# Kernel optimization log

Measured on AMD Instinct MI355X. Metric: run time of the kernel, lower is better.

Reference implementation:

```python
import jax, jax.numpy as jnp
import numpy as np


def _gcn_layer(x, row, col, W, b):
    # x: [N, d_in]; row/col: [E'] (with self loops already appended)
    N = x.shape[0]
    deg = jax.ops.segment_sum(jnp.ones_like(row, dtype=x.dtype), row, num_segments=N)
    deg_inv_sqrt = deg ** -0.5  # self loops guarantee deg >= 1
    norm = deg_inv_sqrt[row] * deg_inv_sqrt[col]  # [E']
    msg = norm[:, None] * x[row]                  # gather + normalize
    aggr = jax.ops.segment_sum(msg, col, num_segments=N)  # scatter-add
    return aggr @ W + b


def reference(x, edge_index, W1, b1, W2, b2):
    N = x.shape[0]
    loops = jnp.arange(N, dtype=edge_index.dtype)
    row = jnp.concatenate([edge_index[0], loops])
    col = jnp.concatenate([edge_index[1], loops])
    h = jax.nn.relu(_gcn_layer(x, row, col, W1, b1))
    # F.dropout(training=self.training) is identity in eval mode
    out = _gcn_layer(h, row, col, W2, b2)
    return jax.nn.log_softmax(out, axis=1)


def setup_inputs() -> dict:
    key = jax.random.key(0)
    k1, k2, k3, k4 = jax.random.split(key, 4)
    N, E, F_IN, F_HID, F_OUT = 100000, 1200000, 64, 64, 16
    x = jax.random.normal(k1, (N, F_IN), dtype=jnp.float32)
    edge_index = jax.random.randint(k2, (2, E), 0, N, dtype=jnp.int64)
    W1 = jax.random.normal(k3, (F_IN, F_HID), dtype=jnp.float32) / np.sqrt(F_IN)
    b1 = jnp.zeros((F_HID,), dtype=jnp.float32)
    W2 = jax.random.normal(k4, (F_HID, F_OUT), dtype=jnp.float32) / np.sqrt(F_HID)
    b2 = jnp.zeros((F_OUT,), dtype=jnp.float32)
    return {"x": x, "edge_index": edge_index, "W1": W1, "b1": b1, "W2": W2, "b2": b2}
```

## Files before the change

### kernel.cpp

```cpp
#include <hip/hip_runtime.h>
#include <hip/hip_bf16.h>

typedef __attribute__((ext_vector_type(8))) _Float16 hfrag;
typedef __attribute__((ext_vector_type(4))) float ffrag;
typedef __attribute__((ext_vector_type(4))) _Float16 h4v;

#define BSH 8
#define LBS 256
#define CAP_SH 14
#define CAP (1 << CAP_SH)
#define NF 512
#define OPAD 520
#define CONV_BLKS 384
#define EPBC 4096
#define ELC 4096

__device__ __forceinline__ float b2f_(unsigned short u) {
    return __uint_as_float(((unsigned)u) << 16);
}
__device__ __forceinline__ unsigned short f2b_(float v) {
    __hip_bfloat16 h = __float2bfloat16(v);
    return *reinterpret_cast<unsigned short*>(&h);
}
__device__ __forceinline__ unsigned short f2h_(float v) {
    _Float16 h = (_Float16)v;
    return __builtin_bit_cast(unsigned short, h);
}
__device__ __forceinline__ float h2f_(unsigned short u) {
    _Float16 h = __builtin_bit_cast(_Float16, u);
    return (float)h;
}

__device__ __forceinline__ float loadF(const void* p, long long i, int isF32) {
    if (isF32) return ((const float*)p)[i];
    return b2f_(((const unsigned short*)p)[i]);
}

__device__ __forceinline__ float4 loadF4(const void* p, long long base, int i4, int isF32) {
    if (isF32) {
        return ((const float4*)((const float*)p + base))[i4];
    } else {
        ushort4 u = ((const ushort4*)((const unsigned short*)p + base))[i4];
        return make_float4(b2f_(u.x), b2f_(u.y), b2f_(u.z), b2f_(u.w));
    }
}

__device__ __forceinline__ void get_edge(const int* ei, int i64, int e, int E, int& s, int& d) {
    if (i64) { s = ei[2 * (long long)e]; d = ei[2 * (long long)E + 2 * (long long)e]; }
    else     { s = ei[e];                d = ei[(long long)E + e]; }
}

struct E4 { int s[4]; int d[4]; };
__device__ __forceinline__ E4 load4(const int* __restrict__ ei, int i64, int e0, int E) {
    E4 r;
    if (i64) {
        const int4* ps = (const int4*)(ei + 2 * (long long)e0);
        const int4* pd = (const int4*)(ei + 2 * (long long)E + 2 * (long long)e0);
        int4 a = ps[0], b = ps[1];
        int4 c = pd[0], d = pd[1];
        r.s[0] = a.x; r.s[1] = a.z; r.s[2] = b.x; r.s[3] = b.z;
        r.d[0] = c.x; r.d[1] = c.z; r.d[2] = d.x; r.d[3] = d.z;
    } else {
        int4 a = *(const int4*)(ei + e0);
        int4 c = *(const int4*)(ei + (long long)E + e0);
        r.s[0] = a.x; r.s[1] = a.y; r.s[2] = a.z; r.s[3] = a.w;
        r.d[0] = c.x; r.d[1] = c.y; r.d[2] = c.z; r.d[3] = c.w;
    }
    return r;
}

__device__ __forceinline__ void wave_scan_excl(int* a, int nEl, int lane) {
    int run = 0;
    for (int base = 0; base < nEl; base += 64) {
        int i = base + lane;
        int orig = (i < nEl) ? a[i] : 0;
        int v = orig;
#pragma unroll
        for (int off = 1; off < 64; off <<= 1) {
            int u = __shfl_up(v, off);
            if (lane >= off) v += u;
        }
        if (i < nEl) a[i] = v - orig + run;
        run += __shfl(v, 63);
    }
}

__global__ __launch_bounds__(256) void k_stage(const void* __restrict__ x,
                                               const int* __restrict__ ei,
                                               const void* __restrict__ W1, const void* __restrict__ b1,
                                               const void* __restrict__ W2, const void* __restrict__ b2,
                                               int E, int N, int nbk, int EPB,
                                               int* __restrict__ flags, float* __restrict__ Wbuf,
                                               unsigned short* __restrict__ Wh1,
                                               unsigned short* __restrict__ Wh2,
                                               int* __restrict__ off_d, int* __restrict__ off_s,
                                               int* __restrict__ pdst,
                                               unsigned char* __restrict__ psrc,
                                               unsigned short* __restrict__ xh) {
    __shared__ int hd[512], hs[512], cd[512], cs[512];
    __shared__ int es[EPBC], ed[EPBC];
    __shared__ int s_sane, s_zero;
    int tid = threadIdx.x;
    if (tid == 0) { s_sane = 0; s_zero = 0; }
    __syncthreads();
    const unsigned short* xu = (const unsigned short*)x;
    if (blockIdx.x == NF) {
        int sane = 0;
        for (int k = tid; k < 4096; k += 256) {
            float v = b2f_(xu[2 * k]);
            float a = fabsf(v);
            if (v == 0.0f || (a >= 9.3e-10f && a <= 1.1e9f)) sane++;
        }
        if (sane) atomicAdd(&s_sane, sane);
        int zero = 0;
        for (int k = tid; k < 1024; k += 256) if (ei[2 * k + 1] == 0) zero++;
        if (zero) atomicAdd(&s_zero, zero);
        __syncthreads();
        int f = (s_sane < 3000) ? 1 : 0;
        if (tid == 0) { flags[0] = f; flags[1] = (s_zero > 512) ? 1 : 0; }
        for (int i = tid; i < 4096; i += 256) Wbuf[i] = loadF(W1, i, f);
        if (tid < 64) Wbuf[4096 + tid] = loadF(b1, tid, f);
        for (int i = tid; i < 1024; i += 256) Wbuf[4160 + i] = loadF(W2, i, f);
        if (tid < 16) Wbuf[5184 + tid] = loadF(b2, tid, f);
        __syncthreads();
        for (int i = tid; i < 4096; i += 256) {
            int j = i & 7, m = (i >> 3) & 15, q = (i >> 7) & 3, kn = i >> 9;
            int kt = kn & 1, nt = kn >> 1;
            Wh1[i] = f2h_(Wbuf[(kt * 32 + q * 8 + j) * 64 + nt * 16 + m]);
        }
        for (int i = tid; i < 1024; i += 256) {
            int j = i & 7, m = (i >> 3) & 15, q = (i >> 7) & 3, kt = i >> 9;
            Wh2[i] = f2h_(Wbuf[4160 + (kt * 32 + q * 8 + j) * 16 + m]);
        }
        return;
    }
    if (blockIdx.x > NF) {
        int cb = blockIdx.x - NF - 1;
        int sane = 0;
        for (int k = tid; k < 4096; k += 256) {
            float v = b2f_(xu[2 * k]);
            float a = fabsf(v);
            if (v == 0.0f || (a >= 9.3e-10f && a <= 1.1e9f)) sane++;
        }
        if (sane) atomicAdd(&s_sane, sane);
        __syncthreads();
        int f = (s_sane < 3000) ? 1 : 0;
        int n4 = N * 16;
        int ctid = cb * 256 + tid;
        int stride = CONV_BLKS * 256 * 2;
        for (int i0 = ctid * 2; i0 < n4; i0 += stride) {
            float4 v0 = loadF4(x, 0, i0, f);
            float4 v1 = (i0 + 1 < n4) ? loadF4(x, 0, i0 + 1, f) : make_float4(0, 0, 0, 0);
            ushort4 o0, o1;
            o0.x = f2h_(v0.x); o0.y = f2h_(v0.y); o0.z = f2h_(v0.z); o0.w = f2h_(v0.w);
            o1.x = f2h_(v1.x); o1.y = f2h_(v1.y); o1.z = f2h_(v1.z); o1.w = f2h_(v1.w);
            ((ushort4*)xh)[i0] = o0;
            if (i0 + 1 < n4) ((ushort4*)xh)[i0 + 1] = o1;
        }
        return;
    }
    int zero = 0;
    for (int k = tid; k < 1024; k += 256) if (ei[2 * k + 1] == 0) zero++;
    if (zero) atomicAdd(&s_zero, zero);
    for (int i = tid; i < 512; i += 256) { hd[i] = 0; hs[i] = 0; }
    __syncthreads();
    int i64 = (s_zero > 512) ? 1 : 0;
    int fb = blockIdx.x;
    int elo = fb * EPB;
    int ehi = min(elo + EPB, E);
    if (elo >= E) {
        for (int b = tid; b <= nbk; b += 256) {
            off_d[fb * OPAD + b] = E; off_s[fb * OPAD + b] = E;
        }
        return;
    }
    int ecnt = ehi - elo;
    int rem = ecnt & 3, ebase = elo + (ecnt & ~3);
    if (ecnt <= EPBC) {
        for (int e0 = elo + tid * 4; e0 + 4 <= ehi; e0 += 1024) {
            E4 a = load4(ei, i64, e0, E);
            int base = e0 - elo;
#pragma unroll
            for (int u = 0; u < 4; ++u) { es[base + u] = a.s[u]; ed[base + u] = a.d[u]; }
        }
        if (tid < rem) {
            int s, d;
            get_edge(ei, i64, ebase + tid, E, s, d);
            es[ecnt - rem + tid] = s; ed[ecnt - rem + tid] = d;
        }
        __syncthreads();
        for (int i = tid; i < ecnt; i += 256) {
            atomicAdd(&hd[ed[i] >> BSH], 1);
            atomicAdd(&hs[es[i] >> BSH], 1);
        }
        __syncthreads();
        if (tid < 64)       wave_scan_excl(hd, nbk, tid);
        else if (tid < 128) wave_scan_excl(hs, nbk, tid - 64);
        __syncthreads();
        for (int b = tid; b < nbk; b += 256) {
            int od = elo + hd[b], os = elo + hs[b];
            off_d[fb * OPAD + b] = od; cd[b] = od;
            off_s[fb * OPAD + b] = os; cs[b] = os;
        }
        if (tid == 0) { off_d[fb * OPAD + nbk] = elo + ecnt; off_s[fb * OPAD + nbk] = elo + ecnt; }
        __syncthreads();
        for (int i = tid; i < ecnt; i += 256) {
            int s = es[i], d = ed[i];
            int p = atomicAdd(&cd[d >> BSH], 1);
            pdst[p] = (s << BSH) | (d & (LBS - 1));
            int q = atomicAdd(&cs[s >> BSH], 1);
            psrc[q] = (unsigned char)(s & (LBS - 1));
        }
        return;
    }
    for (int e0 = elo + tid * 4; e0 + 4 <= ehi; e0 += 1024) {
        E4 a = load4(ei, i64, e0, E);
#pragma unroll
        for (int u = 0; u < 4; ++u) {
            atomicAdd(&hd[a.d[u] >> BSH], 1);
            atomicAdd(&hs[a.s[u] >> BSH], 1);
        }
    }
    if (tid < rem) {
        int s, d;
        get_edge(ei, i64, ebase + tid, E, s, d);
        atomicAdd(&hd[d >> BSH], 1);
        atomicAdd(&hs[s >> BSH], 1);
    }
    __syncthreads();
    if (tid < 64)       wave_scan_excl(hd, nbk, tid);
    else if (tid < 128) wave_scan_excl(hs, nbk, tid - 64);
    __syncthreads();
    for (int b = tid; b < nbk; b += 256) {
        int od = elo + hd[b], os = elo + hs[b];
        off_d[fb * OPAD + b] = od; cd[b] = od;
        off_s[fb * OPAD + b] = os; cs[b] = os;
    }
    if (tid == 0) { off_d[fb * OPAD + nbk] = elo + ecnt; off_s[fb * OPAD + nbk] = elo + ecnt; }
    __syncthreads();
    for (int e0 = elo + tid * 4; e0 + 4 <= ehi; e0 += 1024) {
        E4 a = load4(ei, i64, e0, E);
#pragma unroll
        for (int u = 0; u < 4; ++u) {
            int p = atomicAdd(&cd[a.d[u] >> BSH], 1);
            pdst[p] = (a.s[u] << BSH) | (a.d[u] & (LBS - 1));
            int q = atomicAdd(&cs[a.s[u] >> BSH], 1);
            psrc[q] = (unsigned char)(a.s[u] & (LBS - 1));
        }
    }
    if (tid < rem) {
        int s, d;
        get_edge(ei, i64, ebase + tid, E, s, d);
        int p = atomicAdd(&cd[d >> BSH], 1);
        pdst[p] = (s << BSH) | (d & (LBS - 1));
        int q = atomicAdd(&cs[s >> BSH], 1);
        psrc[q] = (unsigned char)(s & (LBS - 1));
    }
}

__global__ __launch_bounds__(512) void k_degcsr(const unsigned char* __restrict__ psrc,
                                                const int* __restrict__ pdst,
                                                const int* __restrict__ off_s,
                                                const int* __restrict__ off_d,
                                                float* __restrict__ dis,
                                                int4* __restrict__ rdesc,
                                                int* __restrict__ psr, int N, int nbk) {
    __shared__ int elist[ELC];
    __shared__ int h[LBS], lb[LBS], cur[LBS];
    __shared__ float dloc[LBS];
    __shared__ int s_cnt;
    int b = blockIdx.x, tid = threadIdx.x;
    if (tid == 0) s_cnt = 0;
    if (tid < LBS) h[tid] = 0;
    __syncthreads();
    for (int fb = tid; fb < NF; fb += 512) {
        int o0 = off_s[fb * OPAD + b];
        int o1 = off_s[fb * OPAD + b + 1];
        for (int p = o0; p < o1; ++p) atomicAdd(&h[psrc[p]], 1);
    }
    __syncthreads();
    if (tid < LBS) {
        float dv = rsqrtf((float)h[tid] + 1.0f);
        dloc[tid] = dv;
        int node = b * LBS + tid;
        if (node < N) dis[node] = dv;
    }
    __syncthreads();
    if (tid < LBS) h[tid] = 0;
    __syncthreads();
    for (int fb = tid; fb < NF; fb += 512) {
        int o0 = off_d[fb * OPAD + b];
        int o1 = off_d[fb * OPAD + b + 1];
        int len = o1 - o0;
        if (len > 0) {
            int base = atomicAdd(&s_cnt, len);
            for (int k = 0; k < len; ++k)
                if (base + k < ELC) elist[base + k] = pdst[o0 + k];
        }
    }
    __syncthreads();
    int cnt = s_cnt;
    int beg = b << CAP_SH;
    if (cnt <= ELC) {
        for (int i = tid; i < cnt; i += 512) atomicAdd(&h[elist[i] & (LBS - 1)], 1);
        __syncthreads();
        if (tid < LBS) lb[tid] = h[tid];
        __syncthreads();
        if (tid < 64) wave_scan_excl(lb, LBS, tid);
        __syncthreads();
        if (tid < LBS) {
            cur[tid] = lb[tid];
            int node = b * LBS + tid;
            if (node < N) {
                int s0 = min(lb[tid], CAP), s1 = min(lb[tid] + h[tid], CAP);
                rdesc[node] = make_int4(beg + s0, beg + s1, __float_as_int(dloc[tid]), 0);
            }
        }
        __syncthreads();
        for (int i = tid; i < cnt; i += 512) {
            int e = elist[i];
            int r = atomicAdd(&cur[e & (LBS - 1)], 1);
            if (r < CAP) psr[beg + r] = e >> BSH;
        }
        return;
    }
    if (tid < LBS) h[tid] = 0;
    __syncthreads();
    for (int fb = tid; fb < NF; fb += 512) {
        int o0 = off_d[fb * OPAD + b];
        int o1 = off_d[fb * OPAD + b + 1];
        for (int p = o0; p < o1; ++p) atomicAdd(&h[pdst[p] & (LBS - 1)], 1);
    }
    __syncthreads();
    if (tid < LBS) lb[tid] = h[tid];
    __syncthreads();
    if (tid < 64) wave_scan_excl(lb, LBS, tid);
    __syncthreads();
    if (tid < LBS) {
        cur[tid] = lb[tid];
        int node = b * LBS + tid;
        if (node < N) {
            int s0 = min(lb[tid], CAP), s1 = min(lb[tid] + h[tid], CAP);
            rdesc[node] = make_int4(beg + s0, beg + s1, __float_as_int(dloc[tid]), 0);
        }
    }
    __syncthreads();
    for (int fb = tid; fb < NF; fb += 512) {
        int o0 = off_d[fb * OPAD + b];
        int o1 = off_d[fb * OPAD + b + 1];
        for (int p = o0; p < o1; ++p) {
            int e = pdst[p];
            int r = atomicAdd(&cur[e & (LBS - 1)], 1);
            if (r < CAP) psr[beg + r] = e >> BSH;
        }
    }
}

__global__ __launch_bounds__(256) void k_aggdense(const unsigned short* __restrict__ xh,
                                                  const float* __restrict__ dis,
                                                  const int4* __restrict__ rdesc,
                                                  const int* __restrict__ psr,
                                                  const unsigned short* __restrict__ Wh1,
                                                  const unsigned short* __restrict__ Wh2,
                                                  const float* __restrict__ Wbuf,
                                                  unsigned short* __restrict__ t2b, int N) {
    __shared__ __align__(16) unsigned short T[16 * 72];
    int tid = threadIdx.x;
    int lane = tid & 63;
    int w = tid >> 6;
    int g = lane >> 4, i4 = lane & 15;
    int ln = w * 4 + g;
    int n = blockIdx.x * 16 + ln;
    int act = (n < N);
    float4 A[4];
#pragma unroll
    for (int u = 0; u < 4; ++u) A[u] = make_float4(0.f, 0.f, 0.f, 0.f);
    float dd = 0.f;
    int beg = 0, end = 0;
    if (act) {
        int4 rd = rdesc[n];
        beg = rd.x; end = rd.y; dd = __int_as_float(rd.z);
        h4v xv = *(const h4v*)(xh + (long long)n * 64 + i4 * 4);
        float ww = dd * dd;
        A[0].x = ww * (float)xv[0]; A[0].y = ww * (float)xv[1];
        A[0].z = ww * (float)xv[2]; A[0].w = ww * (float)xv[3];
    }
    int cnt = end - beg;
    int Tn = (cnt + 7) >> 3;
    int p = beg;
    int e[8];
#pragma unroll
    for (int u = 0; u < 8; ++u) e[u] = psr[p + u];
    for (int t = 0; t < Tn; ++t) {
        h4v hv[8];
        float dv[8];
#pragma unroll
        for (int u = 0; u < 8; ++u) {
            unsigned ex = min((unsigned)e[u], (unsigned)(N - 1));
            hv[u] = *(const h4v*)(xh + (long long)ex * 64 + i4 * 4);
            dv[u] = dis[ex];
        }
        float nv[8];
#pragma unroll
        for (int u = 0; u < 8; ++u) nv[u] = (p + u < end) ? dd * dv[u] : 0.f;
#pragma unroll
        for (int u = 0; u < 8; ++u) e[u] = psr[p + 8 + u];
        p += 8;
#pragma unroll
        for (int u = 0; u < 8; ++u) {
            A[u & 3].x += nv[u] * (float)hv[u][0];
            A[u & 3].y += nv[u] * (float)hv[u][1];
            A[u & 3].z += nv[u] * (float)hv[u][2];
            A[u & 3].w += nv[u] * (float)hv[u][3];
        }
    }
    float4 s;
    s.x = A[0].x + A[1].x + A[2].x + A[3].x;
    s.y = A[0].y + A[1].y + A[2].y + A[3].y;
    s.z = A[0].z + A[1].z + A[2].z + A[3].z;
    s.w = A[0].w + A[1].w + A[2].w + A[3].w;
    ushort4 o;
    o.x = f2h_(s.x); o.y = f2h_(s.y); o.z = f2h_(s.z); o.w = f2h_(s.w);
    *(ushort4*)(&T[ln * 72 + i4 * 4]) = o;
    __syncthreads();
    int m = lane & 15, q = lane >> 4;
    const unsigned short* arow = &T[m * 72 + q * 8];
    hfrag A0 = *(const hfrag*)(arow);
    hfrag A1 = *(const hfrag*)(arow + 32);
    int nt = w;
    hfrag B0 = *(const hfrag*)(Wh1 + (((nt * 2 + 0) * 4 + q) * 16 + m) * 8);
    hfrag B1 = *(const hfrag*)(Wh1 + (((nt * 2 + 1) * 4 + q) * 16 + m) * 8);
    ffrag z = {0.f, 0.f, 0.f, 0.f};
    z = __builtin_amdgcn_mfma_f32_16x16x32_f16(A0, B0, z, 0, 0, 0);
    z = __builtin_amdgcn_mfma_f32_16x16x32_f16(A1, B1, z, 0, 0, 0);
    float b1n = Wbuf[4096 + nt * 16 + m];
    __syncthreads();
#pragma unroll
    for (int r = 0; r < 4; ++r) {
        float hv = fmaxf(z[r] + b1n, 0.0f);
        T[(q * 4 + r) * 72 + nt * 16 + m] = f2h_(hv);
    }
    __syncthreads();
    if (w == 0) {
        const unsigned short* hrow = &T[m * 72 + q * 8];
        hfrag H0 = *(const hfrag*)(hrow);
        hfrag H1 = *(const hfrag*)(hrow + 32);
        hfrag C0 = *(const hfrag*)(Wh2 + ((0 * 4 + q) * 16 + m) * 8);
        hfrag C1 = *(const hfrag*)(Wh2 + ((1 * 4 + q) * 16 + m) * 8);
        ffrag t2 = {0.f, 0.f, 0.f, 0.f};
        t2 = __builtin_amdgcn_mfma_f32_16x16x32_f16(H0, C0, t2, 0, 0, 0);
        t2 = __builtin_amdgcn_mfma_f32_16x16x32_f16(H1, C1, t2, 0, 0, 0);
#pragma unroll
        for (int r = 0; r < 4; ++r) {
            int nn = blockIdx.x * 16 + q * 4 + r;
            if (nn < N) t2b[(size_t)nn * 16 + m] = f2h_(t2[r]);
        }
    }
}

__global__ __launch_bounds__(256) void k_l2(const unsigned short* __restrict__ t2b,
                                            const int* __restrict__ flags,
                                            const float* __restrict__ dis,
                                            const int4* __restrict__ rdesc,
                                            const int* __restrict__ psr,
                                            const float* __restrict__ Wbuf,
                                            void* __restrict__ out, int N) {
    int isF32 = flags[0];
    int tid = threadIdx.x, lane = tid & 63;
    int g = lane >> 4, i = lane & 15;
    int n = blockIdx.x * 16 + (tid >> 6) * 4 + g;
    if (n >= N) return;
    int4 rd = rdesc[n];
    int beg = rd.x, end = rd.y;
    float dd = __int_as_float(rd.z);
    int cnt = end - beg;
    float A[4];
    A[0] = dd * dd * h2f_(t2b[(size_t)n * 16 + i]);
    A[1] = 0.f; A[2] = 0.f; A[3] = 0.f;
    int T = (cnt + 7) >> 3;
    int p = beg;
    int e[8];
#pragma unroll
    for (int u = 0; u < 8; ++u) e[u] = psr[p + u];
    for (int t = 0; t < T; ++t) {
        float r[8], dv[8];
#pragma unroll
        for (int u = 0; u < 8; ++u) {
            unsigned ex = min((unsigned)e[u], (unsigned)(N - 1));
            r[u] = h2f_(t2b[(size_t)ex * 16 + i]);
            dv[u] = dis[ex];
        }
        float nv[8];
#pragma unroll
        for (int u = 0; u < 8; ++u) nv[u] = (p + u < end) ? dd * dv[u] : 0.f;
#pragma unroll
        for (int u = 0; u < 8; ++u) e[u] = psr[p + 8 + u];
        p += 8;
#pragma unroll
        for (int u = 0; u < 8; ++u) A[u & 3] += nv[u] * r[u];
    }
    float a0 = A[0] + A[1] + A[2] + A[3];
    float v = a0 + Wbuf[5184 + i];
    float mx = v;
#pragma unroll
    for (int off = 8; off; off >>= 1) mx = fmaxf(mx, __shfl_xor(mx, off, 16));
    float ex = __expf(v - mx);
    float ss = ex;
#pragma unroll
    for (int off = 8; off; off >>= 1) ss += __shfl_xor(ss, off, 16);
    float r = v - mx - logf(ss);
    size_t oi = (size_t)n * 16 + i;
    if (isF32) ((float*)out)[oi] = r;
    else       ((unsigned short*)out)[oi] = f2b_(r);
}

extern "C" void kernel_launch(void* const* d_in, const int* in_sizes, int n_in,
                              void* d_out, int out_size, void* d_ws, size_t ws_size,
                              hipStream_t stream) {
    const void* x  = d_in[0];
    const int*  ei = (const int*)d_in[1];
    const void* W1 = d_in[2];
    const void* b1 = d_in[3];
    const void* W2 = d_in[4];
    const void* b2 = d_in[5];

    const int N = in_sizes[0] / 64;
    const int E = in_sizes[1] / 2;
    const int nbk = (N + LBS - 1) >> BSH;
    const int EPB = (((E + NF - 1) / NF) + 7) & ~7;

    char* p = (char*)d_ws;
#define CARVE(ty, name, bytes) ty name = (ty)p; p += (((size_t)(bytes)) + 63) & ~(size_t)63;
    CARVE(int*,   flags,     16)
    CARVE(float*, Wbuf,      5200 * 4)
    CARVE(unsigned short*, Wh1, 4096 * 2)
    CARVE(unsigned short*, Wh2, 1024 * 2)
    CARVE(float*, dis,       (size_t)N * 4)
    CARVE(int4*,  rdesc,     (size_t)N * 16)
    CARVE(int*,   off_d,     (size_t)NF * OPAD * 4)
    CARVE(int*,   off_s,     (size_t)NF * OPAD * 4)
    CARVE(int*,   pdst,      (size_t)NF * EPB * 4)
    CARVE(unsigned char*, psrc, (size_t)NF * EPB)
    CARVE(int*,   psr,       (((size_t)nbk << CAP_SH) + 64) * 4)
    CARVE(unsigned short*, xh,   (size_t)N * 64 * 2)
    CARVE(unsigned short*, t2b,  (size_t)N * 16 * 2)
#undef CARVE

    k_stage<<<NF + 1 + CONV_BLKS, 256, 0, stream>>>(x, ei, W1, b1, W2, b2,
                                                    E, N, nbk, EPB,
                                                    flags, Wbuf, Wh1, Wh2,
                                                    off_d, off_s, pdst, psrc, xh);
    k_degcsr<<<nbk, 512, 0, stream>>>(psrc, pdst, off_s, off_d, dis, rdesc, psr, N, nbk);
    k_aggdense<<<(N + 15) / 16, 256, 0, stream>>>(xh, dis, rdesc, psr,
                                                  Wh1, Wh2, Wbuf, t2b, N);
    k_l2<<<(N + 15) / 16, 256, 0, stream>>>(t2b, flags, dis, rdesc, psr, Wbuf, d_out, N);
}
```

Baseline: 179.8 us.

## Widen per-lane gather vectors so each wave covers more nodes in both aggregations

Layer-1 aggregation now gives each node 8 lanes that each load 8 halves (16 bytes), instead of 16 lanes loading 4 halves. A block now covers 32 nodes and runs two MFMA row tiles. Layer-2 aggregation gives each node 4 lanes that each load ushort4, with the log-softmax reduction done over 4 lanes, so each wave handles 16 nodes. The aim is fewer, wider gather loads and more edges in flight per wave, which should improve latency hiding on the random-access gathers. In exchange each thread holds more registers, lanes are split across nodes with uneven degree so load balance may suffer, and fewer blocks are launched.

```diff
diff --git a/kernel.cpp b/kernel.cpp
--- a/kernel.cpp
+++ b/kernel.cpp
@@ -3,7 +3,6 @@
 
 typedef __attribute__((ext_vector_type(8))) _Float16 hfrag;
 typedef __attribute__((ext_vector_type(4))) float ffrag;
-typedef __attribute__((ext_vector_type(4))) _Float16 h4v;
 
 #define BSH 8
 #define LBS 256
@@ -364,26 +363,27 @@
                                                   const unsigned short* __restrict__ Wh2,
                                                   const float* __restrict__ Wbuf,
                                                   unsigned short* __restrict__ t2b, int N) {
-    __shared__ __align__(16) unsigned short T[16 * 72];
+    __shared__ __align__(16) unsigned short T[32 * 72];
     int tid = threadIdx.x;
     int lane = tid & 63;
     int w = tid >> 6;
-    int g = lane >> 4, i4 = lane & 15;
-    int ln = w * 4 + g;
-    int n = blockIdx.x * 16 + ln;
+    int l8 = lane & 7;
+    int ns = lane >> 3;
+    int ln = w * 8 + ns;
+    int n = blockIdx.x * 32 + ln;
     int act = (n < N);
-    float4 A[4];
-#pragma unroll
-    for (int u = 0; u < 4; ++u) A[u] = make_float4(0.f, 0.f, 0.f, 0.f);
+    float A[8];
+#pragma unroll
+    for (int j = 0; j < 8; ++j) A[j] = 0.f;
     float dd = 0.f;
     int beg = 0, end = 0;
     if (act) {
         int4 rd = rdesc[n];
         beg = rd.x; end = rd.y; dd = __int_as_float(rd.z);
-        h4v xv = *(const h4v*)(xh + (long long)n * 64 + i4 * 4);
+        hfrag xv = *(const hfrag*)(xh + (long long)n * 64 + l8 * 8);
         float ww = dd * dd;
-        A[0].x = ww * (float)xv[0]; A[0].y = ww * (float)xv[1];
-        A[0].z = ww * (float)xv[2]; A[0].w = ww * (float)xv[3];
+#pragma unroll
+        for (int j = 0; j < 8; ++j) A[j] = ww * (float)xv[j];
     }
     int cnt = end - beg;
     int Tn = (cnt + 7) >> 3;
@@ -392,12 +392,12 @@
 #pragma unroll
     for (int u = 0; u < 8; ++u) e[u] = psr[p + u];
     for (int t = 0; t < Tn; ++t) {
-        h4v hv[8];
+        hfrag hv[8];
         float dv[8];
 #pragma unroll
         for (int u = 0; u < 8; ++u) {
             unsigned ex = min((unsigned)e[u], (unsigned)(N - 1));
-            hv[u] = *(const h4v*)(xh + (long long)ex * 64 + i4 * 4);
+            hv[u] = *(const hfrag*)(xh + (long long)ex * 64 + l8 * 8);
             dv[u] = dis[ex];
         }
         float nv[8];
@@ -407,42 +407,45 @@
         for (int u = 0; u < 8; ++u) e[u] = psr[p + 8 + u];
         p += 8;
 #pragma unroll
-        for (int u = 0; u < 8; ++u) {
-            A[u & 3].x += nv[u] * (float)hv[u][0];
-            A[u & 3].y += nv[u] * (float)hv[u][1];
-            A[u & 3].z += nv[u] * (float)hv[u][2];
-            A[u & 3].w += nv[u] * (float)hv[u][3];
-        }
-    }
-    float4 s;
-    s.x = A[0].x + A[1].x + A[2].x + A[3].x;
-    s.y = A[0].y + A[1].y + A[2].y + A[3].y;
-    s.z = A[0].z + A[1].z + A[2].z + A[3].z;
-    s.w = A[0].w + A[1].w + A[2].w + A[3].w;
-    ushort4 o;
-    o.x = f2h_(s.x); o.y = f2h_(s.y); o.z = f2h_(s.z); o.w = f2h_(s.w);
-    *(ushort4*)(&T[ln * 72 + i4 * 4]) = o;
+        for (int u = 0; u < 8; ++u)
+#pragma unroll
+            for (int j = 0; j < 8; ++j)
+                A[j] += nv[u] * (float)hv[u][j];
+    }
+    {
+        ushort4 o0, o1;
+        o0.x = f2h_(A[0]); o0.y = f2h_(A[1]); o0.z = f2h_(A[2]); o0.w = f2h_(A[3]);
+        o1.x = f2h_(A[4]); o1.y = f2h_(A[5]); o1.z = f2h_(A[6]); o1.w = f2h_(A[7]);
+        *(ushort4*)(&T[ln * 72 + l8 * 8]) = o0;
+        *(ushort4*)(&T[ln * 72 + l8 * 8 + 4]) = o1;
+    }
     __syncthreads();
     int m = lane & 15, q = lane >> 4;
-    const unsigned short* arow = &T[m * 72 + q * 8];
-    hfrag A0 = *(const hfrag*)(arow);
-    hfrag A1 = *(const hfrag*)(arow + 32);
     int nt = w;
     hfrag B0 = *(const hfrag*)(Wh1 + (((nt * 2 + 0) * 4 + q) * 16 + m) * 8);
     hfrag B1 = *(const hfrag*)(Wh1 + (((nt * 2 + 1) * 4 + q) * 16 + m) * 8);
-    ffrag z = {0.f, 0.f, 0.f, 0.f};
-    z = __builtin_amdgcn_mfma_f32_16x16x32_f16(A0, B0, z, 0, 0, 0);
-    z = __builtin_amdgcn_mfma_f32_16x16x32_f16(A1, B1, z, 0, 0, 0);
+    const unsigned short* a0row = &T[m * 72 + q * 8];
+    hfrag A00 = *(const hfrag*)(a0row);
+    hfrag A01 = *(const hfrag*)(a0row + 32);
+    const unsigned short* a1row = &T[(16 + m) * 72 + q * 8];
+    hfrag A10 = *(const hfrag*)(a1row);
+    hfrag A11 = *(const hfrag*)(a1row + 32);
+    ffrag z0 = {0.f, 0.f, 0.f, 0.f}, z1 = {0.f, 0.f, 0.f, 0.f};
+    z0 = __builtin_amdgcn_mfma_f32_16x16x32_f16(A00, B0, z0, 0, 0, 0);
+    z0 = __builtin_amdgcn_mfma_f32_16x16x32_f16(A01, B1, z0, 0, 0, 0);
+    z1 = __builtin_amdgcn_mfma_f32_16x16x32_f16(A10, B0, z1, 0, 0, 0);
+    z1 = __builtin_amdgcn_mfma_f32_16x16x32_f16(A11, B1, z1, 0, 0, 0);
     float b1n = Wbuf[4096 + nt * 16 + m];
     __syncthreads();
 #pragma unroll
     for (int r = 0; r < 4; ++r) {
-        float hv = fmaxf(z[r] + b1n, 0.0f);
-        T[(q * 4 + r) * 72 + nt * 16 + m] = f2h_(hv);
-    }
-    __syncthreads();
-    if (w == 0) {
-        const unsigned short* hrow = &T[m * 72 + q * 8];
+        T[(q * 4 + r) * 72 + nt * 16 + m]        = f2h_(fmaxf(z0[r] + b1n, 0.0f));
+        T[(16 + q * 4 + r) * 72 + nt * 16 + m]   = f2h_(fmaxf(z1[r] + b1n, 0.0f));
+    }
+    __syncthreads();
+    if (w < 2) {
+        int mt = w;
+        const unsigned short* hrow = &T[(mt * 16 + m) * 72 + q * 8];
         hfrag H0 = *(const hfrag*)(hrow);
         hfrag H1 = *(const hfrag*)(hrow + 32);
         hfrag C0 = *(const hfrag*)(Wh2 + ((0 * 4 + q) * 16 + m) * 8);
@@ -452,7 +455,7 @@
         t2 = __builtin_amdgcn_mfma_f32_16x16x32_f16(H1, C1, t2, 0, 0, 0);
 #pragma unroll
         for (int r = 0; r < 4; ++r) {
-            int nn = blockIdx.x * 16 + q * 4 + r;
+            int nn = blockIdx.x * 32 + mt * 16 + q * 4 + r;
             if (nn < N) t2b[(size_t)nn * 16 + m] = f2h_(t2[r]);
         }
     }
@@ -467,27 +470,30 @@
                                             void* __restrict__ out, int N) {
     int isF32 = flags[0];
     int tid = threadIdx.x, lane = tid & 63;
-    int g = lane >> 4, i = lane & 15;
-    int n = blockIdx.x * 16 + (tid >> 6) * 4 + g;
+    int i4l = lane & 3;
+    int ns = lane >> 2;
+    int n = blockIdx.x * 64 + (tid >> 6) * 16 + ns;
     if (n >= N) return;
     int4 rd = rdesc[n];
     int beg = rd.x, end = rd.y;
     float dd = __int_as_float(rd.z);
     int cnt = end - beg;
-    float A[4];
-    A[0] = dd * dd * h2f_(t2b[(size_t)n * 16 + i]);
-    A[1] = 0.f; A[2] = 0.f; A[3] = 0.f;
+    ushort4 own = *(const ushort4*)(t2b + (size_t)n * 16 + i4l * 4);
+    float ww = dd * dd;
+    float acc0 = ww * h2f_(own.x), acc1 = ww * h2f_(own.y);
+    float acc2 = ww * h2f_(own.z), acc3 = ww * h2f_(own.w);
     int T = (cnt + 7) >> 3;
     int p = beg;
     int e[8];
 #pragma unroll
     for (int u = 0; u < 8; ++u) e[u] = psr[p + u];
     for (int t = 0; t < T; ++t) {
-        float r[8], dv[8];
+        ushort4 rv[8];
+        float dv[8];
 #pragma unroll
         for (int u = 0; u < 8; ++u) {
             unsigned ex = min((unsigned)e[u], (unsigned)(N - 1));
-            r[u] = h2f_(t2b[(size_t)ex * 16 + i]);
+            rv[u] = *(const ushort4*)(t2b + (size_t)ex * 16 + i4l * 4);
             dv[u] = dis[ex];
         }
         float nv[8];
@@ -497,21 +503,33 @@
         for (int u = 0; u < 8; ++u) e[u] = psr[p + 8 + u];
         p += 8;
 #pragma unroll
-        for (int u = 0; u < 8; ++u) A[u & 3] += nv[u] * r[u];
-    }
-    float a0 = A[0] + A[1] + A[2] + A[3];
-    float v = a0 + Wbuf[5184 + i];
-    float mx = v;
-#pragma unroll
-    for (int off = 8; off; off >>= 1) mx = fmaxf(mx, __shfl_xor(mx, off, 16));
-    float ex = __expf(v - mx);
-    float ss = ex;
-#pragma unroll
-    for (int off = 8; off; off >>= 1) ss += __shfl_xor(ss, off, 16);
-    float r = v - mx - logf(ss);
-    size_t oi = (size_t)n * 16 + i;
-    if (isF32) ((float*)out)[oi] = r;
-    else       ((unsigned short*)out)[oi] = f2b_(r);
+        for (int u = 0; u < 8; ++u) {
+            acc0 += nv[u] * h2f_(rv[u].x);
+            acc1 += nv[u] * h2f_(rv[u].y);
+            acc2 += nv[u] * h2f_(rv[u].z);
+            acc3 += nv[u] * h2f_(rv[u].w);
+        }
+    }
+    float v0 = acc0 + Wbuf[5184 + i4l * 4 + 0];
+    float v1 = acc1 + Wbuf[5184 + i4l * 4 + 1];
+    float v2 = acc2 + Wbuf[5184 + i4l * 4 + 2];
+    float v3 = acc3 + Wbuf[5184 + i4l * 4 + 3];
+    float mx = fmaxf(fmaxf(v0, v1), fmaxf(v2, v3));
+    mx = fmaxf(mx, __shfl_xor(mx, 1, 4));
+    mx = fmaxf(mx, __shfl_xor(mx, 2, 4));
+    float ss = __expf(v0 - mx) + __expf(v1 - mx) + __expf(v2 - mx) + __expf(v3 - mx);
+    ss += __shfl_xor(ss, 1, 4);
+    ss += __shfl_xor(ss, 2, 4);
+    float ls = logf(ss);
+    float r0 = v0 - mx - ls, r1 = v1 - mx - ls, r2 = v2 - mx - ls, r3 = v3 - mx - ls;
+    size_t oi = (size_t)n * 16 + i4l * 4;
+    if (isF32) {
+        *(float4*)((float*)out + oi) = make_float4(r0, r1, r2, r3);
+    } else {
+        ushort4 o;
+        o.x = f2b_(r0); o.y = f2b_(r1); o.z = f2b_(r2); o.w = f2b_(r3);
+        *(ushort4*)((unsigned short*)out + oi) = o;
+    }
 }
 
 extern "C" void kernel_launch(void* const* d_in, const int* in_sizes, int n_in,
@@ -551,7 +569,7 @@
                                                     flags, Wbuf, Wh1, Wh2,
                                                     off_d, off_s, pdst, psrc, xh);
     k_degcsr<<<nbk, 512, 0, stream>>>(psrc, pdst, off_s, off_d, dis, rdesc, psr, N, nbk);
-    k_aggdense<<<(N + 15) / 16, 256, 0, stream>>>(xh, dis, rdesc, psr,
+    k_aggdense<<<(N + 31) / 32, 256, 0, stream>>>(xh, dis, rdesc, psr,
                                                   Wh1, Wh2, Wbuf, t2b, N);
-    k_l2<<<(N + 15) / 16, 256, 0, stream>>>(t2b, flags, dis, rdesc, psr, Wbuf, d_out, N);
-}
+    k_l2<<<(N + 63) / 64, 256, 0, stream>>>(t2b, flags, dis, rdesc, psr, Wbuf, d_out, N);
+}
```

Result: slower. 183.9 us (+2.3%).
